# Performance work log

Hardware: AMD Instinct MI355X
Metric: run time of the kernel (lower is better)

The kernel has to match this reference:

```python
import jax, jax.numpy as jnp
import numpy as np
from jax import lax

SD = 16  # sample_duration
POOL_KS = (SD, SD * 3 // 4, SD // 2, SD // 4)  # (16, 12, 8, 4)


def conv3d_same(x, w, b):
    # x: [B,C,T,H,W], w: [O,I,3,3,3]
    y = lax.conv_general_dilated(
        x, w, window_strides=(1, 1, 1), padding=[(1, 1), (1, 1), (1, 1)],
        dimension_numbers=("NCDHW", "OIDHW", "NCDHW"))
    return y + b[None, :, None, None, None]


def maxpool_t(x, k):
    # MaxPool3d((k,1,1), stride=1): max over sliding temporal window
    return lax.reduce_window(x, -jnp.inf, lax.max,
                             (1, 1, k, 1, 1), (1, 1, 1, 1, 1), "VALID")


def head1x1(x, w, b):
    # 1x1x1 Conv3d as einsum; x: [B,C,T,H,W], w: [O,C]
    return jnp.einsum("bcthw,oc->bothw", x, w) + b[None, :, None, None, None]


def cls_prob(score):
    # _RPN.reshape(x,2) -> softmax(dim=1) -> reshape back to [B,30,T,H,W]
    B, C, T, H, W = score.shape
    s2 = score.reshape(B, 2, (C * T) // 2, H, W)
    p = jax.nn.softmax(s2, axis=1)
    return p.reshape(B, C, T, H, W)


def setup_inputs() -> dict:
    key = jax.random.key(0)
    ks = jax.random.split(key, 12)
    din, B, H, W = 512, 2, 28, 28
    s = 0.05
    return {
        "base_feat": jax.random.normal(ks[0], (B, din, SD, H, W), jnp.float32),
        "im_info": jnp.ones((B, 3), jnp.float32) * 448.0,
        "gt_boxes": jax.random.uniform(ks[1], (B, 20, 5), jnp.float32),
        "gt_rois": jax.random.uniform(ks[2], (B, 20, SD, 5), jnp.float32),
        "W_conv": jax.random.normal(ks[3], (din, din, 3, 3, 3), jnp.float32) * 0.01,
        "b_conv": jnp.zeros((din,), jnp.float32),
        "W_cls": jax.random.normal(ks[4], (30, din), jnp.float32) * s,
        "b_cls": jnp.zeros((30,), jnp.float32),
        "W_bbox": jax.random.normal(ks[5], (960, din), jnp.float32) * s,
        "b_bbox": jnp.zeros((960,), jnp.float32),
        "W_bbox_34": jax.random.normal(ks[6], (720, din), jnp.float32) * s,
        "b_bbox_34": jnp.zeros((720,), jnp.float32),
        "W_bbox_2": jax.random.normal(ks[7], (480, din), jnp.float32) * s,
        "b_bbox_2": jnp.zeros((480,), jnp.float32),
        "W_bbox_4": jax.random.normal(ks[8], (240, din), jnp.float32) * s,
        "b_bbox_4": jnp.zeros((240,), jnp.float32),
    }


def reference(base_feat, im_info, gt_boxes, gt_rois,
              W_conv, b_conv, W_cls, b_cls,
              W_bbox, b_bbox, W_bbox_34, b_bbox_34,
              W_bbox_2, b_bbox_2, W_bbox_4, b_bbox_4):
    # RPN conv + relu
    x = jax.nn.relu(conv3d_same(base_feat, W_conv, b_conv))
    # four temporal max-pool branches (T' = 1, 5, 9, 13)
    pools = [maxpool_t(x, k) for k in POOL_KS]
    # NOTE: original code applies the SAME RPN_cls_score conv to all branches
    probs = tuple(cls_prob(head1x1(p, W_cls, b_cls)) for p in pools)
    bbox_ws = [(W_bbox, b_bbox), (W_bbox_34, b_bbox_34),
               (W_bbox_2, b_bbox_2), (W_bbox_4, b_bbox_4)]
    bboxes = tuple(head1x1(p, w, b) for p, (w, b) in zip(pools, bbox_ws))
    return probs + bboxes
```

## Files before the change

### kernel.cpp

```cpp
#include <hip/hip_runtime.h>

typedef unsigned short u16;
typedef unsigned int   u32;
typedef __bf16  bf16x8 __attribute__((ext_vector_type(8)));
typedef float   f32x4  __attribute__((ext_vector_type(4)));

__device__ __forceinline__ float bf2f(u16 u) {
    u32 v = ((u32)u) << 16;
    return __builtin_bit_cast(float, v);
}
__device__ __forceinline__ u16 f2bf(float f) {
    u32 u = __builtin_bit_cast(u32, f);
    return (u16)((u + 0x7FFFu + ((u >> 16) & 1u)) >> 16);
}
__device__ __forceinline__ float ldf(const void* p, long i, int f32) {
    return f32 ? ((const float*)p)[i] : bf2f(((const u16*)p)[i]);
}
__device__ __forceinline__ int is_f32(const u32* im) {
    return im[0] == 0x43E00000u;
}
__device__ __forceinline__ void gl2lds16(const u16* g, u16* l) {
    __builtin_amdgcn_global_load_lds(
        (const __attribute__((address_space(1))) void*)g,
        (__attribute__((address_space(3))) void*)l, 16, 0, 0);
}

__global__ void zero_kernel(uint4* __restrict__ p, const int n)
{
    int i = blockIdx.x * 256 + threadIdx.x;
    if (i < n) p[i] = uint4{0u, 0u, 0u, 0u};
}

__global__ void pad_fill(const void* __restrict__ src, u16* __restrict__ xpad,
                         const u32* __restrict__ im)
{
    const int f32 = is_f32(im);
    __shared__ u16 lds[56 * 40];
    int blk = blockIdx.x;
    const int h2  = blk % 14;  blk /= 14;
    const int c32 = blk & 15;  blk >>= 4;
    const int t   = blk & 15;
    const int b   = blk >> 4;
    const int tid = threadIdx.x;
    const long sbase = ((long)(b * 512 + c32 * 32) * 16 + t) * 784 + h2 * 56;
    #pragma unroll
    for (int it = tid; it < 1792; it += 256) {
        const int c = it / 56, p = it - c * 56;
        float v = f32 ? ((const float*)src)[sbase + (long)c * 12544 + p]
                      : bf2f(((const u16*)src)[sbase + (long)c * 12544 + p]);
        lds[p * 40 + c] = f2bf(v);
    }
    __syncthreads();
    if (tid < 224) {
        const int p = tid >> 2, g = tid & 3;
        const int h = h2 * 2 + p / 28, w = p % 28;
        const long o = (((long)(b * 18 + t + 1) * 30 + h + 1) * 30 + (w + 1)) * 512
                       + c32 * 32 + g * 8;
        *(uint4*)&xpad[o] = *(const uint4*)&lds[p * 40 + g * 8];
    }
}

__global__ void wt_transform(const void* __restrict__ wconv, u16* __restrict__ wt,
                             const u32* __restrict__ im)
{
    const int f32 = is_f32(im);
    __shared__ u16 lds[256 * 28];
    const int tid = threadIdx.x;
    const int pair_base = blockIdx.x * 256;
    const long s0 = (long)pair_base * 27;
    for (int it = tid; it < 256 * 27; it += 256) {
        const int p = it / 27, o = it - p * 27;
        float v = f32 ? ((const float*)wconv)[s0 + it]
                      : bf2f(((const u16*)wconv)[s0 + it]);
        lds[p * 28 + o] = f2bf(v);
    }
    __syncthreads();
    #pragma unroll
    for (int off = 0; off < 27; ++off)
        wt[(long)off * 262144 + pair_base + tid] = lds[tid * 28 + off];
}

__global__ void cvt_all(const void* s0, const void* s1, const void* s2,
                        const void* s3, const void* s4,
                        const void* b0, const void* b1, const void* b2,
                        const void* b3, const void* b4, const void* b5,
                        u16* __restrict__ whd, float* __restrict__ bfs,
                        const u32* __restrict__ im)
{
    const int f32 = is_f32(im);
    int i = blockIdx.x * 256 + threadIdx.x;
    if (i < 1244160) {
        const void* s; long j;
        if      (i < 15360)   { s = s0; j = i; }
        else if (i < 506880)  { s = s1; j = i - 15360; }
        else if (i < 875520)  { s = s2; j = i - 506880; }
        else if (i < 1121280) { s = s3; j = i - 875520; }
        else                  { s = s4; j = i - 1121280; }
        whd[i] = f2bf(ldf(s, j, f32));
        return;
    }
    i -= 1244160;
    if (i >= 2942) return;
    float v;
    if      (i < 512)  v = ldf(b0, i, f32);
    else if (i < 542)  v = ldf(b1, i - 512, f32);
    else if (i < 1502) v = ldf(b2, i - 542, f32);
    else if (i < 2222) v = ldf(b3, i - 1502, f32);
    else if (i < 2702) v = ldf(b4, i - 2222, f32);
    else               v = ldf(b5, i - 2702, f32);
    bfs[i] = v;
}

__global__ __launch_bounds__(512, 2) void conv_gemm256(
    const u16* __restrict__ xpad, const u16* __restrict__ wt,
    const float* __restrict__ bfs, u16* __restrict__ y)
{
    __shared__ u16 smem[65536];
    const int tid = threadIdx.x;

    const int bx  = blockIdx.x;
    const int xcd = bx & 7, pos = bx >> 3;
    const int L   = (xcd < 4 ? xcd * 25 : 100 + (xcd - 4) * 24) + pos;
    const int m_base = (L & 1) * 256;
    const int n_base = (L >> 1) * 256;

    const int rq  = tid >> 2;
    const int gsw = (((tid & 3) ^ ((tid >> 3) & 3))) * 8;
    const u16* pa0 = wt + (long)(m_base + rq) * 512 + gsw;
    const u16* pa1 = pa0 + 128 * 512;

    const int n0 = n_base + rq;
    const int n1 = n0 + 128;
    int b0 = n0 / 12544, r0 = n0 % 12544;
    int t0 = r0 / 784,   q0 = r0 % 784;
    int h0 = q0 / 28,    w0 = q0 % 28;
    int b1 = n1 / 12544, r1 = n1 % 12544;
    int t1 = r1 / 784,   q1 = r1 % 784;
    int h1 = q1 / 28,    w1 = q1 % 28;
    const int sa0 = ((b0 * 18 + t0) * 30 + h0) * 30 + w0;
    const int sa1 = ((b1 * 18 + t1) * 30 + h1) * 30 + w1;
    const u16* pb0 = xpad + (long)sa0 * 512 + gsw;
    const u16* pb1 = xpad + (long)sa1 * 512 + gsw;

    const int lane = tid & 63, wid = tid >> 6;
    const int l16 = lane & 15, quad = lane >> 4;
    const int wm = wid >> 2;
    const int wn = wid & 3;
    const int slot  = (quad ^ ((l16 >> 1) & 3)) * 8;
    const int aoffs = (wm * 128 + l16) * 32 + slot;
    const int boffs = 8192 + (wn * 64 + l16) * 32 + slot;

    f32x4 acc[8][4] = {};

    #pragma unroll
    for (int k = 0; k < 3; ++k) {
        u16* dst = smem + (k << 14);
        gl2lds16(pa0 + k * 32, dst + tid * 8);
        gl2lds16(pa1 + k * 32, dst + 4096  + tid * 8);
        gl2lds16(pb0 + k * 32, dst + 8192  + tid * 8);
        gl2lds16(pb1 + k * 32, dst + 12288 + tid * 8);
    }

#define KTILE(ktl, STG, GATE)                                                  \
    {                                                                          \
        asm volatile("s_waitcnt vmcnt(" #GATE ")" ::: "memory");               \
        asm volatile("s_barrier" ::: "memory");                                \
        const u16* buf = smem + (((ktl) & 3) << 14);                           \
        bf16x8 af[8], bfr[4];                                                  \
        _Pragma("unroll")                                                      \
        for (int mi = 0; mi < 4; ++mi)                                         \
            af[mi] = *(const bf16x8*)&buf[aoffs + mi * 512];                   \
        _Pragma("unroll")                                                      \
        for (int ni = 0; ni < 4; ++ni)                                         \
            bfr[ni] = *(const bf16x8*)&buf[boffs + ni * 512];                  \
        _Pragma("unroll")                                                      \
        for (int mi = 4; mi < 8; ++mi)                                         \
            af[mi] = *(const bf16x8*)&buf[aoffs + mi * 512];                   \
        if (STG) {                                                             \
            const int kts = (ktl) + 3;                                         \
            const int tap = kts >> 4, kc = kts & 15;                           \
            const int kd = tap / 9, r9 = tap - kd * 9;                         \
            const int kh = r9 / 3,  kw = r9 - kh * 3;                          \
            const long aoff = (long)tap * 262144 + kc * 32;                    \
            const long boff = (long)(kd * 900 + kh * 30 + kw) * 512 + kc * 32; \
            u16* dst = smem + ((kts & 3) << 14);                               \
            gl2lds16(pa0 + aoff, dst + tid * 8);                               \
            gl2lds16(pa1 + aoff, dst + 4096  + tid * 8);                       \
            gl2lds16(pb0 + boff, dst + 8192  + tid * 8);                       \
            gl2lds16(pb1 + boff, dst + 12288 + tid * 8);                       \
        }                                                                      \
        __builtin_amdgcn_s_setprio(1);                                         \
        _Pragma("unroll")                                                      \
        for (int mi = 0; mi < 4; ++mi)                                         \
            _Pragma("unroll")                                                  \
            for (int ni = 0; ni < 4; ++ni)                                     \
                acc[mi][ni] = __builtin_amdgcn_mfma_f32_16x16x32_bf16(         \
                    af[mi], bfr[ni], acc[mi][ni], 0, 0, 0);                    \
        _Pragma("unroll")                                                      \
        for (int mi = 4; mi < 8; ++mi)                                         \
            _Pragma("unroll")                                                  \
            for (int ni = 0; ni < 4; ++ni)                                     \
                acc[mi][ni] = __builtin_amdgcn_mfma_f32_16x16x32_bf16(         \
                    af[mi], bfr[ni], acc[mi][ni], 0, 0, 0);                    \
        __builtin_amdgcn_s_setprio(0);                                         \
    }

    for (int kt = 0; kt < 429; ++kt) KTILE(kt, 1, 8)
    KTILE(429, 0, 8)
    KTILE(430, 0, 4)
    KTILE(431, 0, 0)
#undef KTILE

    #pragma unroll
    for (int mi = 0; mi < 8; ++mi) {
        const int mrow = m_base + wm * 128 + mi * 16 + quad * 4;
        float bias[4];
        #pragma unroll
        for (int r = 0; r < 4; ++r) bias[r] = bfs[mrow + r];
        #pragma unroll
        for (int ni = 0; ni < 4; ++ni) {
            const int ng = n_base + wn * 64 + ni * 16 + l16;
            f32x4 a = acc[mi][ni];
            u16 o0 = f2bf(fmaxf(a[0] + bias[0], 0.f));
            u16 o1 = f2bf(fmaxf(a[1] + bias[1], 0.f));
            u16 o2 = f2bf(fmaxf(a[2] + bias[2], 0.f));
            u16 o3 = f2bf(fmaxf(a[3] + bias[3], 0.f));
            uint2 pv;
            pv.x = (u32)o0 | ((u32)o1 << 16);
            pv.y = (u32)o2 | ((u32)o3 << 16);
            *(uint2*)&y[(long)ng * 512 + mrow] = pv;
        }
    }
}

__device__ __forceinline__ uint2 max4(uint2 A, uint2 Bv)
{
    const u16* a = (const u16*)&A;
    const u16* b = (const u16*)&Bv;
    uint2 R;
    u16* r = (u16*)&R;
    #pragma unroll
    for (int i = 0; i < 4; ++i) r[i] = (bf2f(a[i]) >= bf2f(b[i])) ? a[i] : b[i];
    return R;
}

__global__ void pool_all(const u16* __restrict__ y, u16* __restrict__ p4,
                         u16* __restrict__ p8, u16* __restrict__ p12,
                         u16* __restrict__ p16)
{
    int g = blockIdx.x * 256 + threadIdx.x;
    if (g >= 200704) return;
    const int c4 = g & 127;
    int pos = g >> 7;
    const int hw = pos % 784; const int b = pos / 784;
    const u16* src = y + ((long)(b * 16) * 784 + hw) * 512 + c4 * 4;
    uint2 v[16];
    #pragma unroll
    for (int t = 0; t < 16; ++t)
        v[t] = *(const uint2*)(src + (long)t * 401408);
    uint2 pr[15];
    #pragma unroll
    for (int t = 0; t < 15; ++t) pr[t] = max4(v[t], v[t + 1]);
    uint2 qd[13];
    #pragma unroll
    for (int t = 0; t < 13; ++t) qd[t] = max4(pr[t], pr[t + 2]);
    uint2 e8[9];
    #pragma unroll
    for (int t = 0; t < 9; ++t) e8[t] = max4(qd[t], qd[t + 4]);
    uint2 e12[5];
    #pragma unroll
    for (int t = 0; t < 5; ++t) e12[t] = max4(e8[t], qd[t + 8]);
    uint2 e16 = max4(e8[0], e8[8]);

    const long col = (long)hw * 512 + c4 * 4;
    #pragma unroll
    for (int t = 0; t < 13; ++t)
        *(uint2*)&p4[((long)(b * 13 + t) * 784) * 512 + col] = qd[t];
    #pragma unroll
    for (int t = 0; t < 9; ++t)
        *(uint2*)&p8[((long)(b * 9 + t) * 784) * 512 + col] = e8[t];
    #pragma unroll
    for (int t = 0; t < 5; ++t)
        *(uint2*)&p12[((long)(b * 5 + t) * 784) * 512 + col] = e12[t];
    *(uint2*)&p16[((long)b * 784) * 512 + col] = e16;
}

__global__ __launch_bounds__(256, 2) void heads_gemm(
    const u16* __restrict__ p16, const u16* __restrict__ p12,
    const u16* __restrict__ p8,  const u16* __restrict__ p4,
    const u16* __restrict__ wcls, const u16* __restrict__ wb1,
    const u16* __restrict__ wb34, const u16* __restrict__ wb2,
    const u16* __restrict__ wb4,  const float* __restrict__ bfs,
    float* __restrict__ clsr, void* __restrict__ outv,
    const u32* __restrict__ im)
{
    const int f32 = is_f32(im);
    int bid = blockIdx.x;
    const u16* pool; const u16* wbp; int Ti, CH, nt, mt; long boff, coff, ooff;
    if (bid < 104)      {             nt = bid % 13;  mt = bid / 13;  pool = p16; wbp = wb1;  Ti = 1;  CH = 960; boff = 542;  coff = 0;      ooff = 1317120; }
    else if (bid < 476) { bid -= 104; nt = bid % 62;  mt = bid / 62;  pool = p12; wbp = wb34; Ti = 5;  CH = 720; boff = 1502; coff = 47040;  ooff = 2822400; }
    else if (bid < 920) { bid -= 476; nt = bid % 111; mt = bid / 111; pool = p8;  wbp = wb2;  Ti = 9;  CH = 480; boff = 2222; coff = 282240; ooff = 8467200; }
    else                { bid -= 920; nt = bid % 160; mt = bid / 160; pool = p4;  wbp = wb4;  Ti = 13; CH = 240; boff = 2702; coff = 705600; ooff = 15240960; }
    const int M = 30 + CH;
    const int THW = Ti * 784;
    const int N = 2 * THW;
    const int n_base = nt * 128;
    const int m_base = mt * 128;

    __shared__ u16 lds_a[128 * 64];
    __shared__ u16 lds_b[128 * 64];
    const int tid = threadIdx.x;
    const int lane = tid & 63;
    const int wid  = tid >> 6;
    const int quad = lane >> 4;
    const int l16  = lane & 15;
    const int wm = (wid & 1) * 64;
    const int wn = (wid >> 1) * 64;
    const int srow = tid >> 3;
    const int lc8  = ((tid & 7) ^ (srow & 7)) * 8;

    const u16* arow[4]; const u16* brow[4];
    #pragma unroll
    for (int j = 0; j < 4; ++j) {
        int m = m_base + j * 32 + srow; if (m > M - 1) m = M - 1;
        arow[j] = ((m < 30) ? (wcls + m * 512) : (wbp + (m - 30) * 512)) + lc8;
        int n = n_base + j * 32 + srow; if (n > N - 1) n = N - 1;
        brow[j] = pool + (long)n * 512 + lc8;
    }

    u16* ldst_a = &lds_a[tid * 8];
    u16* ldst_b = &lds_b[tid * 8];

    int rowA[4], rowB[4];
    #pragma unroll
    for (int i = 0; i < 4; ++i) {
        rowA[i] = (wm + i * 16 + l16) * 64;
        rowB[i] = (wn + i * 16 + l16) * 64;
    }
    const int cx  = l16 & 7;
    const int ch0 = (quad ^ cx) * 8;
    const int ch1 = ((4 + quad) ^ cx) * 8;

    f32x4 acc[4][4] = {};
    for (int kc = 0; kc < 8; ++kc) {
        const int kcol = kc * 64;
        #pragma unroll
        for (int j = 0; j < 4; ++j)
            gl2lds16(arow[j] + kcol, ldst_a + j * 2048);
        #pragma unroll
        for (int j = 0; j < 4; ++j)
            gl2lds16(brow[j] + kcol, ldst_b + j * 2048);
        __syncthreads();
        #pragma unroll
        for (int h = 0; h < 2; ++h) {
            const int co = h ? ch1 : ch0;
            bf16x8 af[4], bfr[4];
            #pragma unroll
            for (int mi = 0; mi < 4; ++mi)
                af[mi]  = *(const bf16x8*)&lds_a[rowA[mi] + co];
            #pragma unroll
            for (int ni = 0; ni < 4; ++ni)
                bfr[ni] = *(const bf16x8*)&lds_b[rowB[ni] + co];
            #pragma unroll
            for (int mi = 0; mi < 4; ++mi)
                #pragma unroll
                for (int ni = 0; ni < 4; ++ni)
                    acc[mi][ni] = __builtin_amdgcn_mfma_f32_16x16x32_bf16(
                        af[mi], bfr[ni], acc[mi][ni], 0, 0, 0);
        }
        __syncthreads();
    }
    const float* bcls = bfs + 512;
    const float* bb   = bfs + boff;
    #pragma unroll
    for (int mi = 0; mi < 4; ++mi) {
        const int mrow = m_base + wm + mi * 16 + quad * 4;
        #pragma unroll
        for (int ni = 0; ni < 4; ++ni) {
            const int ng = n_base + wn + ni * 16 + l16;
            if (ng >= N) continue;
            const int b  = ng / THW;
            const int rr = ng % THW;
            f32x4 a = acc[mi][ni];
            #pragma unroll
            for (int r = 0; r < 4; ++r) {
                const int m = mrow + r;
                if (m >= M) break;
                const float bias = (m < 30) ? bcls[m] : bb[m - 30];
                const float v = a[r] + bias;
                if (m < 30) {
                    clsr[coff + ((long)(b * 30 + m)) * THW + rr] = v;
                } else {
                    const long oi = ooff + ((long)(b * CH + (m - 30))) * THW + rr;
                    if (f32) ((float*)outv)[oi] = v;
                    else     ((u16*)outv)[oi]   = f2bf(v);
                }
            }
        }
    }
}

__global__ void softmax_all(const float* __restrict__ clsr,
                            void* __restrict__ outv, const u32* __restrict__ im)
{
    const int f32 = is_f32(im);
    int g = blockIdx.x * 256 + threadIdx.x;
    if (g >= 658560) return;
    int Ti; long off;
    if      (g < 23520)  { Ti = 1;  off = 0; }
    else if (g < 141120) { Ti = 5;  off = 47040;  g -= 23520; }
    else if (g < 352800) { Ti = 9;  off = 282240; g -= 141120; }
    else                 { Ti = 13; off = 705600; g -= 352800; }
    const int THW = Ti * 784;
    const int rr = g % THW;
    int r2 = g / THW;
    const int j = r2 % 15; const int b = r2 / 15;
    const long i0 = off + ((long)(b * 30 + j)) * THW + rr;
    const long i1 = off + ((long)(b * 30 + j + 15)) * THW + rr;
    const float s0 = clsr[i0], s1 = clsr[i1];
    const float mx = fmaxf(s0, s1);
    const float e0 = __expf(s0 - mx), e1 = __expf(s1 - mx);
    const float inv = 1.0f / (e0 + e1);
    if (f32) {
        ((float*)outv)[i0] = e0 * inv;
        ((float*)outv)[i1] = e1 * inv;
    } else {
        ((u16*)outv)[i0] = f2bf(e0 * inv);
        ((u16*)outv)[i1] = f2bf(e1 * inv);
    }
}

extern "C" void kernel_launch(void* const* d_in, const int* in_sizes, int n_in,
                              void* d_out, int out_size, void* d_ws, size_t ws_size,
                              hipStream_t stream)
{
    const void* base_feat = d_in[0];
    const u32*  im_info   = (const u32*)d_in[1];
    const void* W_conv    = d_in[4];
    const void* b_conv    = d_in[5];
    const void* W_cls     = d_in[6];
    const void* b_cls     = d_in[7];
    const void* W_bbox    = d_in[8];
    const void* b_bbox    = d_in[9];
    const void* W_bbox34  = d_in[10];
    const void* b_bbox34  = d_in[11];
    const void* W_bbox2   = d_in[12];
    const void* b_bbox2   = d_in[13];
    const void* W_bbox4   = d_in[14];
    const void* b_bbox4   = d_in[15];

    char* ws = (char*)d_ws;
    u16*   xpad = (u16*)  (ws + 0);
    u16*   wt   = (u16*)  (ws + 33177600);
    u16*   y    = (u16*)  (ws + 47333376);
    u16*   p4   = (u16*)  (ws + 73023488);
    u16*   p8   = (u16*)  (ws + 93896704);
    u16*   p12  = (u16*)  (ws + 108347392);
    u16*   p16  = (u16*)  (ws + 116375552);
    float* clsr = (float*)(ws + 117981184);
    u16*   whd  = (u16*)  (ws + 123249728);
    float* bfs  = (float*)(ws + 125738048);

    u16* w_cls_b  = whd;
    u16* w_b1_b   = whd + 15360;
    u16* w_b34_b  = whd + 506880;
    u16* w_b2_b   = whd + 875520;
    u16* w_b4_b   = whd + 1121280;

    zero_kernel<<<8100, 256, 0, stream>>>((uint4*)xpad, 2073600);
    pad_fill<<<7168, 256, 0, stream>>>(base_feat, xpad, im_info);
    wt_transform<<<1024, 256, 0, stream>>>(W_conv, wt, im_info);
    cvt_all<<<4873, 256, 0, stream>>>(W_cls, W_bbox, W_bbox34, W_bbox2, W_bbox4,
                                      b_conv, b_cls, b_bbox, b_bbox34, b_bbox2,
                                      b_bbox4, whd, bfs, im_info);

    conv_gemm256<<<196, 512, 0, stream>>>(xpad, wt, bfs, y);

    pool_all<<<784, 256, 0, stream>>>(y, p4, p8, p12, p16);

    heads_gemm<<<1400, 256, 0, stream>>>(p16, p12, p8, p4,
                                         w_cls_b, w_b1_b, w_b34_b, w_b2_b, w_b4_b,
                                         bfs, clsr, d_out, im_info);

    softmax_all<<<2573, 256, 0, stream>>>(clsr, d_out, im_info);
}
```

Before: 571.6 us.

## Use 64-wide K tiles with double buffering in conv GEMM; zero only padding halo

The conv implicit GEMM now loads 64-element K tiles into two 64KB LDS buffers instead of 32-element tiles in a four-deep ring. This halves the number of barriers and wait points and issues two MFMA rounds per tile. It uses a new 8-way XOR swizzle to avoid LDS bank conflicts. The cost is a shallower prefetch: the loop waits for all outstanding loads (vmcnt 0) every iteration. Separately, the full-buffer zero kernel is replaced by one that writes only the halo cells of the padded input, cutting redundant memory writes.

Measured after the change: 573.1 us. About the same (+0.3%).

```diff
diff --git a/kernel.cpp b/kernel.cpp
--- a/kernel.cpp
+++ b/kernel.cpp
@@ -25,10 +25,36 @@
         (__attribute__((address_space(3))) void*)l, 16, 0, 0);
 }
 
-__global__ void zero_kernel(uint4* __restrict__ p, const int n)
+__global__ void zero_halo(u16* __restrict__ xpad)
 {
     int i = blockIdx.x * 256 + threadIdx.x;
-    if (i < n) p[i] = uint4{0u, 0u, 0u, 0u};
+    if (i < 230400) {
+        int c8 = i & 63; int pos = i >> 6;
+        int p = pos % 900; pos /= 900;
+        int t = (pos & 1) * 17; int b = pos >> 1;
+        long o = (((long)(b * 18 + t) * 900) + p) * 512 + c8 * 8;
+        *(uint4*)&xpad[o] = uint4{0u, 0u, 0u, 0u};
+        return;
+    }
+    i -= 230400;
+    if (i < 122880) {
+        int c8 = i & 63; int pos = i >> 6;
+        int w = pos % 30; pos /= 30;
+        int h = (pos & 1) * 29; pos >>= 1;
+        int t = pos % 16 + 1; int b = pos / 16;
+        long o = ((((long)(b * 18 + t) * 30 + h) * 30) + w) * 512 + c8 * 8;
+        *(uint4*)&xpad[o] = uint4{0u, 0u, 0u, 0u};
+        return;
+    }
+    i -= 122880;
+    if (i < 114688) {
+        int c8 = i & 63; int pos = i >> 6;
+        int w = (pos & 1) * 29; pos >>= 1;
+        int h = pos % 28 + 1; pos /= 28;
+        int t = pos % 16 + 1; int b = pos / 16;
+        long o = ((((long)(b * 18 + t) * 30 + h) * 30) + w) * 512 + c8 * 8;
+        *(uint4*)&xpad[o] = uint4{0u, 0u, 0u, 0u};
+    }
 }
 
 __global__ void pad_fill(const void* __restrict__ src, u16* __restrict__ xpad,
@@ -124,92 +150,104 @@
     const int m_base = (L & 1) * 256;
     const int n_base = (L >> 1) * 256;
 
-    const int rq  = tid >> 2;
-    const int gsw = (((tid & 3) ^ ((tid >> 3) & 3))) * 8;
-    const u16* pa0 = wt + (long)(m_base + rq) * 512 + gsw;
-    const u16* pa1 = pa0 + 128 * 512;
-
-    const int n0 = n_base + rq;
-    const int n1 = n0 + 128;
-    int b0 = n0 / 12544, r0 = n0 % 12544;
-    int t0 = r0 / 784,   q0 = r0 % 784;
-    int h0 = q0 / 28,    w0 = q0 % 28;
-    int b1 = n1 / 12544, r1 = n1 % 12544;
-    int t1 = r1 / 784,   q1 = r1 % 784;
-    int h1 = q1 / 28,    w1 = q1 % 28;
-    const int sa0 = ((b0 * 18 + t0) * 30 + h0) * 30 + w0;
-    const int sa1 = ((b1 * 18 + t1) * 30 + h1) * 30 + w1;
-    const u16* pb0 = xpad + (long)sa0 * 512 + gsw;
-    const u16* pb1 = xpad + (long)sa1 * 512 + gsw;
+    const int rq8 = tid >> 3;
+    const int sw  = (((tid & 7) ^ (rq8 & 7))) * 8;
+    const u16* pa = wt + (long)(m_base + rq8) * 512 + sw;
+
+    long sbj[4];
+    #pragma unroll
+    for (int j = 0; j < 4; ++j) {
+        const int n = n_base + j * 64 + rq8;
+        int b = n / 12544, r = n % 12544;
+        int t = r / 784,   q = r % 784;
+        int h = q / 28,    w = q % 28;
+        const int sa = ((b * 18 + t) * 30 + h) * 30 + w;
+        sbj[j] = (long)sa * 512 + sw;
+    }
 
     const int lane = tid & 63, wid = tid >> 6;
     const int l16 = lane & 15, quad = lane >> 4;
     const int wm = wid >> 2;
     const int wn = wid & 3;
-    const int slot  = (quad ^ ((l16 >> 1) & 3)) * 8;
-    const int aoffs = (wm * 128 + l16) * 32 + slot;
-    const int boffs = 8192 + (wn * 64 + l16) * 32 + slot;
+    const int x7 = l16 & 7;
+    const int o0 = (quad ^ x7) * 8;
+    const int o1 = ((4 + quad) ^ x7) * 8;
+    int rowA[8], rowB[4];
+    #pragma unroll
+    for (int mi = 0; mi < 8; ++mi) rowA[mi] = (wm * 128 + mi * 16 + l16) * 64;
+    #pragma unroll
+    for (int ni = 0; ni < 4; ++ni) rowB[ni] = 16384 + (wn * 64 + ni * 16 + l16) * 64;
 
     f32x4 acc[8][4] = {};
 
-    #pragma unroll
-    for (int k = 0; k < 3; ++k) {
-        u16* dst = smem + (k << 14);
-        gl2lds16(pa0 + k * 32, dst + tid * 8);
-        gl2lds16(pa1 + k * 32, dst + 4096  + tid * 8);
-        gl2lds16(pb0 + k * 32, dst + 8192  + tid * 8);
-        gl2lds16(pb1 + k * 32, dst + 12288 + tid * 8);
-    }
-
-#define KTILE(ktl, STG, GATE)                                                  \
-    {                                                                          \
-        asm volatile("s_waitcnt vmcnt(" #GATE ")" ::: "memory");               \
-        asm volatile("s_barrier" ::: "memory");                                \
-        const u16* buf = smem + (((ktl) & 3) << 14);                           \
-        bf16x8 af[8], bfr[4];                                                  \
-        _Pragma("unroll")                                                      \
-        for (int mi = 0; mi < 4; ++mi)                                         \
-            af[mi] = *(const bf16x8*)&buf[aoffs + mi * 512];                   \
-        _Pragma("unroll")                                                      \
-        for (int ni = 0; ni < 4; ++ni)                                         \
-            bfr[ni] = *(const bf16x8*)&buf[boffs + ni * 512];                  \
-        _Pragma("unroll")                                                      \
-        for (int mi = 4; mi < 8; ++mi)                                         \
-            af[mi] = *(const bf16x8*)&buf[aoffs + mi * 512];                   \
-        if (STG) {                                                             \
-            const int kts = (ktl) + 3;                                         \
-            const int tap = kts >> 4, kc = kts & 15;                           \
-            const int kd = tap / 9, r9 = tap - kd * 9;                         \
-            const int kh = r9 / 3,  kw = r9 - kh * 3;                          \
-            const long aoff = (long)tap * 262144 + kc * 32;                    \
-            const long boff = (long)(kd * 900 + kh * 30 + kw) * 512 + kc * 32; \
-            u16* dst = smem + ((kts & 3) << 14);                               \
-            gl2lds16(pa0 + aoff, dst + tid * 8);                               \
-            gl2lds16(pa1 + aoff, dst + 4096  + tid * 8);                       \
-            gl2lds16(pb0 + boff, dst + 8192  + tid * 8);                       \
-            gl2lds16(pb1 + boff, dst + 12288 + tid * 8);                       \
-        }                                                                      \
-        __builtin_amdgcn_s_setprio(1);                                         \
-        _Pragma("unroll")                                                      \
-        for (int mi = 0; mi < 4; ++mi)                                         \
-            _Pragma("unroll")                                                  \
-            for (int ni = 0; ni < 4; ++ni)                                     \
-                acc[mi][ni] = __builtin_amdgcn_mfma_f32_16x16x32_bf16(         \
-                    af[mi], bfr[ni], acc[mi][ni], 0, 0, 0);                    \
-        _Pragma("unroll")                                                      \
-        for (int mi = 4; mi < 8; ++mi)                                         \
-            _Pragma("unroll")                                                  \
-            for (int ni = 0; ni < 4; ++ni)                                     \
-                acc[mi][ni] = __builtin_amdgcn_mfma_f32_16x16x32_bf16(         \
-                    af[mi], bfr[ni], acc[mi][ni], 0, 0, 0);                    \
-        __builtin_amdgcn_s_setprio(0);                                         \
-    }
-
-    for (int kt = 0; kt < 429; ++kt) KTILE(kt, 1, 8)
-    KTILE(429, 0, 8)
-    KTILE(430, 0, 4)
-    KTILE(431, 0, 0)
-#undef KTILE
+    {
+        u16* dst = smem;
+        #pragma unroll
+        for (int j = 0; j < 4; ++j)
+            gl2lds16(pa + (long)j * 32768, dst + j * 4096 + tid * 8);
+        #pragma unroll
+        for (int j = 0; j < 4; ++j)
+            gl2lds16(xpad + sbj[j], dst + 16384 + j * 4096 + tid * 8);
+    }
+
+    for (int kt = 0; kt < 216; ++kt) {
+        asm volatile("s_waitcnt vmcnt(0)" ::: "memory");
+        asm volatile("s_barrier" ::: "memory");
+        const u16* buf = smem + (kt & 1) * 32768;
+
+        bf16x8 af[8], bfr[4];
+        #pragma unroll
+        for (int mi = 0; mi < 4; ++mi)
+            af[mi] = *(const bf16x8*)&buf[rowA[mi] + o0];
+        #pragma unroll
+        for (int ni = 0; ni < 4; ++ni)
+            bfr[ni] = *(const bf16x8*)&buf[rowB[ni] + o0];
+        #pragma unroll
+        for (int mi = 4; mi < 8; ++mi)
+            af[mi] = *(const bf16x8*)&buf[rowA[mi] + o0];
+
+        if (kt < 215) {
+            const int kts = kt + 1;
+            const int tap = kts >> 3, kc = kts & 7;
+            const int kd = tap / 9, r9 = tap - kd * 9;
+            const int kh = r9 / 3,  kw = r9 - kh * 3;
+            const long aoff = (long)tap * 262144 + kc * 64;
+            const long boff = (long)(kd * 900 + kh * 30 + kw) * 512 + kc * 64;
+            u16* dst = smem + ((kts & 1) << 15);
+            #pragma unroll
+            for (int j = 0; j < 4; ++j)
+                gl2lds16(pa + aoff + (long)j * 32768, dst + j * 4096 + tid * 8);
+            #pragma unroll
+            for (int j = 0; j < 4; ++j)
+                gl2lds16(xpad + sbj[j] + boff, dst + 16384 + j * 4096 + tid * 8);
+        }
+
+        __builtin_amdgcn_s_setprio(1);
+        #pragma unroll
+        for (int mi = 0; mi < 8; ++mi)
+            #pragma unroll
+            for (int ni = 0; ni < 4; ++ni)
+                acc[mi][ni] = __builtin_amdgcn_mfma_f32_16x16x32_bf16(
+                    af[mi], bfr[ni], acc[mi][ni], 0, 0, 0);
+        __builtin_amdgcn_s_setprio(0);
+
+        bf16x8 ag[8], bgr[4];
+        #pragma unroll
+        for (int mi = 0; mi < 8; ++mi)
+            ag[mi] = *(const bf16x8*)&buf[rowA[mi] + o1];
+        #pragma unroll
+        for (int ni = 0; ni < 4; ++ni)
+            bgr[ni] = *(const bf16x8*)&buf[rowB[ni] + o1];
+
+        __builtin_amdgcn_s_setprio(1);
+        #pragma unroll
+        for (int mi = 0; mi < 8; ++mi)
+            #pragma unroll
+            for (int ni = 0; ni < 4; ++ni)
+                acc[mi][ni] = __builtin_amdgcn_mfma_f32_16x16x32_bf16(
+                    ag[mi], bgr[ni], acc[mi][ni], 0, 0, 0);
+        __builtin_amdgcn_s_setprio(0);
+    }
 
     #pragma unroll
     for (int mi = 0; mi < 8; ++mi) {
@@ -221,13 +259,13 @@
         for (int ni = 0; ni < 4; ++ni) {
             const int ng = n_base + wn * 64 + ni * 16 + l16;
             f32x4 a = acc[mi][ni];
-            u16 o0 = f2bf(fmaxf(a[0] + bias[0], 0.f));
-            u16 o1 = f2bf(fmaxf(a[1] + bias[1], 0.f));
-            u16 o2 = f2bf(fmaxf(a[2] + bias[2], 0.f));
-            u16 o3 = f2bf(fmaxf(a[3] + bias[3], 0.f));
+            u16 o0v = f2bf(fmaxf(a[0] + bias[0], 0.f));
+            u16 o1v = f2bf(fmaxf(a[1] + bias[1], 0.f));
+            u16 o2v = f2bf(fmaxf(a[2] + bias[2], 0.f));
+            u16 o3v = f2bf(fmaxf(a[3] + bias[3], 0.f));
             uint2 pv;
-            pv.x = (u32)o0 | ((u32)o1 << 16);
-            pv.y = (u32)o2 | ((u32)o3 << 16);
+            pv.x = (u32)o0v | ((u32)o1v << 16);
+            pv.y = (u32)o2v | ((u32)o3v << 16);
             *(uint2*)&y[(long)ng * 512 + mrow] = pv;
         }
     }
@@ -467,7 +505,7 @@
     u16* w_b2_b   = whd + 875520;
     u16* w_b4_b   = whd + 1121280;
 
-    zero_kernel<<<8100, 256, 0, stream>>>((uint4*)xpad, 2073600);
+    zero_halo<<<1828, 256, 0, stream>>>(xpad);
     pad_fill<<<7168, 256, 0, stream>>>(base_feat, xpad, im_info);
     wt_transform<<<1024, 256, 0, stream>>>(W_conv, wt, im_info);
     cvt_all<<<4873, 256, 0, stream>>>(W_cls, W_bbox, W_bbox34, W_bbox2, W_bbox4,
```
